# Optimization experiments

Measured on AMD Instinct MI355X. Metric: run time of the kernel, lower is better.

The kernel has to match this reference:

```python
import jax, jax.numpy as jnp
import numpy as np
from jax import lax

K = 3
STRIDE = 1
PAD = 1


def setup_inputs() -> dict:
    key = jax.random.key(0)
    k0, k1, k2, k3 = jax.random.split(key, 4)
    B, C, H, W, O = 8, 128, 64, 64, 128
    x = jax.random.normal(k0, (B, C, H, W), jnp.float32)
    # offset_conv: Conv2d(C, 2*K*K) - small init so sampled offsets stay moderate
    w_off = jax.random.normal(k1, (2 * K * K, C, K, K), jnp.float32) * 0.01
    b_off = jnp.zeros((2 * K * K,), jnp.float32)
    # deform_conv main weight, kaiming-ish scale
    w_def = jax.random.normal(k2, (O, C, K, K), jnp.float32) * (1.0 / np.sqrt(C * K * K))
    b_def = jax.random.normal(k3, (O,), jnp.float32) * 0.01
    return {"x": x, "w_off": w_off, "b_off": b_off, "w_def": w_def, "b_def": b_def}


def _conv2d(x, w, b, stride, pad):
    y = lax.conv_general_dilated(
        x, w, window_strides=(stride, stride), padding=[(pad, pad), (pad, pad)],
        dimension_numbers=("NCHW", "OIHW", "NCHW"))
    return y + b[None, :, None, None]


def _bilinear_sample(x, py, px):
    """x: [B,C,Hin,Win]; py,px: [B,KK,H,W] -> [B,C,KK,H,W] with zero padding."""
    B, C, Hin, Win = x.shape
    iy0f = jnp.floor(py)
    ix0f = jnp.floor(px)
    wy = py - iy0f  # grad of floor is 0, so d(wy)/d(py) = 1 (matches deform conv)
    wx = px - ix0f
    iy0 = iy0f.astype(jnp.int32)
    ix0 = ix0f.astype(jnp.int32)

    def gather(iy, ix):
        valid = (iy >= 0) & (iy < Hin) & (ix >= 0) & (ix < Win)
        iyc = jnp.clip(iy, 0, Hin - 1)
        ixc = jnp.clip(ix, 0, Win - 1)
        g = jax.vmap(lambda xb, a, b: xb[:, a, b])(x, iyc, ixc)  # [B,C,KK,H,W]
        return g * valid[:, None].astype(x.dtype)

    v00 = gather(iy0, ix0)
    v01 = gather(iy0, ix0 + 1)
    v10 = gather(iy0 + 1, ix0)
    v11 = gather(iy0 + 1, ix0 + 1)
    wy_ = wy[:, None]
    wx_ = wx[:, None]
    return (v00 * (1 - wy_) * (1 - wx_) + v01 * (1 - wy_) * wx_
            + v10 * wy_ * (1 - wx_) + v11 * wy_ * wx_)


def reference(x, w_off, b_off, w_def, b_def):
    B, C, H, W = x.shape
    O = w_def.shape[0]
    KK = K * K
    # 1) standard conv predicting offsets: [B, 2*KK, Hout, Wout]
    offsets = _conv2d(x, w_off, b_off, STRIDE, PAD)
    Hout, Wout = offsets.shape[2], offsets.shape[3]
    # torchvision layout: interleaved (dy, dx) per kernel tap
    off = offsets.reshape(B, KK, 2, Hout, Wout)
    off_y, off_x = off[:, :, 0], off[:, :, 1]  # [B,KK,Hout,Wout]
    # 2) base sampling grid per kernel tap
    kys, kxs = jnp.meshgrid(jnp.arange(K), jnp.arange(K), indexing="ij")
    kys = kys.reshape(KK).astype(jnp.float32)
    kxs = kxs.reshape(KK).astype(jnp.float32)
    hs = (jnp.arange(Hout) * STRIDE - PAD).astype(jnp.float32)
    ws = (jnp.arange(Wout) * STRIDE - PAD).astype(jnp.float32)
    base_y = hs[None, :, None] + kys[:, None, None]  # [KK,Hout,1]
    base_x = ws[None, None, :] + kxs[:, None, None]  # [KK,1,Wout]
    py = base_y[None] + off_y  # [B,KK,Hout,Wout]
    px = base_x[None] + off_x
    # 3) gather bilinear-sampled patches then dense contraction (im2col GEMM)
    sampled = _bilinear_sample(x, py, px)  # [B,C,KK,Hout,Wout]
    out = jnp.einsum("bckhw,ock->bohw", sampled, w_def.reshape(O, C, KK))
    return out + b_def[None, :, None, None]
```

## Files before the change

kernel.cpp:

```cpp
#include <hip/hip_runtime.h>
#include <hip/hip_bf16.h>

#define BB 8
#define CC 128
#define HH 64
#define WW 64
#define OO 128
#define NJ 18
#define HW 4096

typedef unsigned short u16;
typedef unsigned int u32;
typedef __attribute__((ext_vector_type(8))) __bf16 bf16x8;
typedef __attribute__((ext_vector_type(4))) float f32x4;

__device__ __forceinline__ u16 f2bf(float f) {
    u32 u = __float_as_uint(f);
    u += 0x7fffu + ((u >> 16) & 1u);
    return (u16)(u >> 16);
}
__device__ __forceinline__ float bflo(u32 u) { return __uint_as_float(u << 16); }
__device__ __forceinline__ float bfhi(u32 u) { return __uint_as_float(u & 0xffff0000u); }
__device__ __forceinline__ u32 pk2bf(float s0, float s1) {
    union { __hip_bfloat162 h; u32 u; } cv;
    cv.h = __float22bfloat162_rn(make_float2(s0, s1));
    return cv.u;
}

__global__ __launch_bounds__(256)
void k_xT(const float* __restrict__ x, u16* __restrict__ xT) {
    __shared__ float tile[64][129];
    const int t = threadIdx.x;
    const int b = blockIdx.x >> 6;
    const int hw0 = (blockIdx.x & 63) << 6;
    const float* xb = x + (size_t)b * CC * HW + hw0;
    const int tw = t & 63, tc = t >> 6;
#pragma unroll
    for (int r = 0; r < 32; ++r) {
        int c = r * 4 + tc;
        tile[tw][c] = xb[c * HW + tw];
    }
    __syncthreads();
    u16* dst = xT + ((size_t)b * HW + hw0) * CC;
#pragma unroll
    for (int r = 0; r < 4; ++r) {
        int item = t + (r << 8);
        int seg = item & 15, hw = item >> 4;
        union { u32 d[4]; uint4 v; } p;
#pragma unroll
        for (int i = 0; i < 4; ++i)
            p.d[i] = pk2bf(tile[hw][seg * 8 + 2 * i], tile[hw][seg * 8 + 2 * i + 1]);
        *(uint4*)&dst[hw * CC + seg * 8] = p.v;
    }
}

__global__ void k_prep(const float* __restrict__ w_def,
                       const float* __restrict__ w_off,
                       u16* __restrict__ wT, u16* __restrict__ wA) {
    int idx = blockIdx.x * 256 + threadIdx.x;
    if (idx < 9 * OO * CC) {
        int c = idx & 127, o = (idx >> 7) & 127, kk = idx >> 14;
        wT[idx] = f2bf(w_def[(o * CC + c) * 9 + kk]);
    }
    if (idx < 32 * 1152) {
        int k = idx % 1152, j = idx / 1152;
        int q = k >> 7, c = k & 127;
        wA[idx] = (j < NJ) ? f2bf(w_off[(j * CC + c) * 9 + q]) : (u16)0;
    }
}

__global__ __launch_bounds__(256, 2)
void k_off(const u16* __restrict__ xT, const u16* __restrict__ wA,
           const float* __restrict__ b_off, float* __restrict__ offs) {
    __shared__ u16 s_x[198 * 128];
    const int t = threadIdx.x, lane = t & 63, wv = t >> 6;
    const int posl = lane & 15, kg = lane >> 4;
    const int b = blockIdx.x & 7, h = blockIdx.x >> 3;

    for (int it = t; it < 3168; it += 256) {
        int seg = it & 15, pix = it >> 4;
        int r = pix / 66, wp = pix - r * 66;
        int y = h - 1 + r, w = wp - 1;
        uint4 v = make_uint4(0, 0, 0, 0);
        if (y >= 0 && y < HH && w >= 0 && w < WW)
            v = *(const uint4*)&xT[((size_t)(b * HW) + y * WW + w) * CC + seg * 8];
        *(uint4*)&s_x[pix * 128 + ((seg ^ (pix & 15)) * 8)] = v;
    }
    __syncthreads();

    f32x4 acc0 = {0.f, 0.f, 0.f, 0.f}, acc1 = {0.f, 0.f, 0.f, 0.f};
    for (int q = 0; q < 9; ++q) {
        int qy = q / 3, qx = q - qy * 3;
        int pix = qy * 66 + (wv * 16 + posl) + qx;
        int prow = pix * 128, pxor = pix & 15;
#pragma unroll
        for (int ki = 0; ki < 4; ++ki) {
            int ks = q * 4 + ki;
            int cidx = ki * 4 + kg;
            bf16x8 bfr = *(const bf16x8*)&s_x[prow + ((cidx ^ pxor) * 8)];
            bf16x8 a0 = *(const bf16x8*)&wA[posl * 1152 + ks * 32 + kg * 8];
            bf16x8 a1 = *(const bf16x8*)&wA[(16 + posl) * 1152 + ks * 32 + kg * 8];
            acc0 = __builtin_amdgcn_mfma_f32_16x16x32_bf16(a0, bfr, acc0, 0, 0, 0);
            acc1 = __builtin_amdgcn_mfma_f32_16x16x32_bf16(a1, bfr, acc1, 0, 0, 0);
        }
    }
    const int pos = wv * 16 + posl;
#pragma unroll
    for (int r = 0; r < 4; ++r) {
        int j = kg * 4 + r;
        offs[(b * NJ + j) * HW + h * WW + pos] = acc0[r] + b_off[j];
    }
#pragma unroll
    for (int r = 0; r < 4; ++r) {
        int j = 16 + kg * 4 + r;
        if (j < NJ) offs[(b * NJ + j) * HW + h * WW + pos] = acc1[r] + b_off[j];
    }
}

__global__ __launch_bounds__(256, 2)
void k_main(const u16* __restrict__ xT, const float* __restrict__ offs,
            const u16* __restrict__ wT, const float* __restrict__ b_def,
            float* __restrict__ out) {
    __shared__ u16 s_samp[2][64 * 128];

    const int t = threadIdx.x, lane = t & 63, wv = t >> 6;
    const int posl = lane & 15, kg = lane >> 4;
    const int b = blockIdx.x & 7;
    const int h = blockIdx.x >> 3;
    const char* xb = (const char*)xT + (size_t)b * (HW * CC * 2);

    const int gpos = t >> 2;
    const int segsub = t & 3;
    const int pxor = gpos & 15;
    const int slotbase = gpos * 128;

    float oyv[9], oxv[9];
#pragma unroll
    for (int kk = 0; kk < 9; ++kk) {
        oyv[kk] = offs[(b * NJ + 2 * kk) * HW + h * WW + gpos];
        oxv[kk] = offs[(b * NJ + 2 * kk + 1) * HW + h * WW + gpos];
    }

    auto coords = [&](int kk, float oy, float ox, float4& cw, int4& co) {
        int ky = kk / 3, kx = kk - ky * 3;
        float py = (float)(h - 1 + ky) + oy;
        float px = (float)(gpos - 1 + kx) + ox;
        float fy = floorf(py), fx = floorf(px);
        int iy0 = (int)fy, ix0 = (int)fx;
        float wy = py - fy, wx = px - fx;
        int iy1 = iy0 + 1, ix1 = ix0 + 1;
        float my0 = (iy0 >= 0 && iy0 < HH) ? 1.0f : 0.0f;
        float my1 = (iy1 >= 0 && iy1 < HH) ? 1.0f : 0.0f;
        float mx0 = (ix0 >= 0 && ix0 < WW) ? 1.0f : 0.0f;
        float mx1 = (ix1 >= 0 && ix1 < WW) ? 1.0f : 0.0f;
        int iy0c = min(max(iy0, 0), HH - 1), iy1c = min(max(iy1, 0), HH - 1);
        int ix0c = min(max(ix0, 0), WW - 1), ix1c = min(max(ix1, 0), WW - 1);
        float wy1 = 1.0f - wy, wx1 = 1.0f - wx;
        cw = make_float4(my0 * mx0 * wy1 * wx1, my0 * mx1 * wy1 * wx,
                         my1 * mx0 * wy  * wx1, my1 * mx1 * wy  * wx);
        co = make_int4((iy0c * WW + ix0c) << 8, (iy0c * WW + ix1c) << 8,
                       (iy1c * WW + ix0c) << 8, (iy1c * WW + ix1c) << 8);
    };
    auto issue_gather = [&](const int4 co, uint4 q[4][4]) {
#pragma unroll
        for (int j = 0; j < 4; ++j) {
            const int sb = (segsub + 4 * j) * 16;
            q[j][0] = *(const uint4*)(xb + co.x + sb);
            q[j][1] = *(const uint4*)(xb + co.y + sb);
            q[j][2] = *(const uint4*)(xb + co.z + sb);
            q[j][3] = *(const uint4*)(xb + co.w + sb);
        }
    };
    auto interp_store = [&](const float4 cw, uint4 q[4][4], int p) {
#pragma unroll
        for (int j = 0; j < 4; ++j) {
            const int seg = segsub + 4 * j;
            const u32* u00 = (const u32*)&q[j][0];
            const u32* u01 = (const u32*)&q[j][1];
            const u32* u10 = (const u32*)&q[j][2];
            const u32* u11 = (const u32*)&q[j][3];
            union { u32 d[4]; uint4 v; } pk;
#pragma unroll
            for (int i = 0; i < 4; ++i) {
                float s0 = cw.x * bflo(u00[i]) + cw.y * bflo(u01[i])
                         + cw.z * bflo(u10[i]) + cw.w * bflo(u11[i]);
                float s1 = cw.x * bfhi(u00[i]) + cw.y * bfhi(u01[i])
                         + cw.z * bfhi(u10[i]) + cw.w * bfhi(u11[i]);
                pk.d[i] = pk2bf(s0, s1);
            }
            *(uint4*)&s_samp[p][slotbase + ((seg ^ pxor) * 8)] = pk.v;
        }
    };
    auto load_w = [&](int kk, bf16x8 wfr[4][2]) {
        const u16* wkk = wT + kk * (OO * CC);
        const int o0 = wv * 32;
#pragma unroll
        for (int ct = 0; ct < 4; ++ct)
#pragma unroll
            for (int nt = 0; nt < 2; ++nt) {
                int o = o0 + nt * 16 + posl;
                wfr[ct][nt] = *(const bf16x8*)&wkk[o * CC + ct * 32 + kg * 8];
            }
    };

    f32x4 acc[4][2];
#pragma unroll
    for (int mt = 0; mt < 4; ++mt) {
        acc[mt][0] = (f32x4){0.f, 0.f, 0.f, 0.f};
        acc[mt][1] = (f32x4){0.f, 0.f, 0.f, 0.f};
    }

    bf16x8 wA_[4][2], wB_[4][2];
    float4 cw; int4 co;
    uint4 q[4][4];
    load_w(0, wA_);
    coords(0, oyv[0], oxv[0], cw, co);
    issue_gather(co, q);
    interp_store(cw, q, 0);
    __syncthreads();

#pragma unroll
    for (int kk = 0; kk < 9; ++kk) {
        const int p = kk & 1;

        if (kk < 8) {
            load_w(kk + 1, wB_);
            coords(kk + 1, oyv[kk + 1], oxv[kk + 1], cw, co);
            issue_gather(co, q);
        }

#pragma unroll
        for (int ct = 0; ct < 4; ++ct) {
            const int chunk = ct * 4 + kg;
#pragma unroll
            for (int mt = 0; mt < 4; ++mt) {
                bf16x8 afr = *(const bf16x8*)
                    &s_samp[p][(mt * 16 + posl) * 128 + ((chunk ^ posl) * 8)];
                acc[mt][0] = __builtin_amdgcn_mfma_f32_16x16x32_bf16(
                    afr, wA_[ct][0], acc[mt][0], 0, 0, 0);
                acc[mt][1] = __builtin_amdgcn_mfma_f32_16x16x32_bf16(
                    afr, wA_[ct][1], acc[mt][1], 0, 0, 0);
            }
        }

        if (kk < 8) {
            interp_store(cw, q, p ^ 1);
            __syncthreads();
        }

#pragma unroll
        for (int ct = 0; ct < 4; ++ct) {
            wA_[ct][0] = wB_[ct][0];
            wA_[ct][1] = wB_[ct][1];
        }
    }

#pragma unroll
    for (int nt = 0; nt < 2; ++nt) {
        const int o = wv * 32 + nt * 16 + posl;
        const float bd = b_def[o];
        float* orow = out + ((b * OO + o) * HH + h) * WW;
#pragma unroll
        for (int mt = 0; mt < 4; ++mt) {
            float4 res;
            res.x = acc[mt][nt][0] + bd;
            res.y = acc[mt][nt][1] + bd;
            res.z = acc[mt][nt][2] + bd;
            res.w = acc[mt][nt][3] + bd;
            *(float4*)&orow[mt * 16 + kg * 4] = res;
        }
    }
}

extern "C" void kernel_launch(void* const* d_in, const int* in_sizes, int n_in,
                              void* d_out, int out_size, void* d_ws, size_t ws_size,
                              hipStream_t stream) {
    const float* x     = (const float*)d_in[0];
    const float* w_off = (const float*)d_in[1];
    const float* b_off = (const float*)d_in[2];
    const float* w_def = (const float*)d_in[3];
    const float* b_def = (const float*)d_in[4];
    float* out = (float*)d_out;

    float* offs = (float*)d_ws;
    u16*   xT   = (u16*)(offs + BB * NJ * HW);
    u16*   wT   = xT + (size_t)BB * HW * CC;
    u16*   wA   = wT + 9 * OO * CC;

    k_xT  <<<512, 256, 0, stream>>>(x, xT);
    k_prep<<<576, 256, 0, stream>>>(w_def, w_off, wT, wA);
    k_off <<<512, 256, 0, stream>>>(xT, wA, b_off, offs);
    k_main<<<512, 256, 0, stream>>>(xT, offs, wT, b_def, out);
}
```

Baseline: 131.7 us.

## Fuse offset conv into main deform kernel and merge prep kernels

Merges the x transpose and weight prep kernels into one launch, with the block range selecting the role. Fuses the offset convolution into the main deformable-conv kernel: each block computes its row's offsets, keeps them in shared memory (aliased over the halo tile), and then runs the gather/GEMM. This removes two kernel launches and the global round trip for the offsets. In exchange the larger shared footprint and the extra work per block may lower occupancy.

```diff
diff --git a/kernel.cpp b/kernel.cpp
--- a/kernel.cpp
+++ b/kernel.cpp
@@ -28,54 +28,60 @@
 }
 
 __global__ __launch_bounds__(256)
-void k_xT(const float* __restrict__ x, u16* __restrict__ xT) {
+void k_pre(const float* __restrict__ x, u16* __restrict__ xT,
+           const float* __restrict__ w_def, const float* __restrict__ w_off,
+           u16* __restrict__ wT, u16* __restrict__ wA) {
     __shared__ float tile[64][129];
     const int t = threadIdx.x;
-    const int b = blockIdx.x >> 6;
-    const int hw0 = (blockIdx.x & 63) << 6;
-    const float* xb = x + (size_t)b * CC * HW + hw0;
-    const int tw = t & 63, tc = t >> 6;
-#pragma unroll
-    for (int r = 0; r < 32; ++r) {
-        int c = r * 4 + tc;
-        tile[tw][c] = xb[c * HW + tw];
-    }
-    __syncthreads();
-    u16* dst = xT + ((size_t)b * HW + hw0) * CC;
-#pragma unroll
-    for (int r = 0; r < 4; ++r) {
-        int item = t + (r << 8);
-        int seg = item & 15, hw = item >> 4;
-        union { u32 d[4]; uint4 v; } p;
-#pragma unroll
-        for (int i = 0; i < 4; ++i)
-            p.d[i] = pk2bf(tile[hw][seg * 8 + 2 * i], tile[hw][seg * 8 + 2 * i + 1]);
-        *(uint4*)&dst[hw * CC + seg * 8] = p.v;
-    }
-}
-
-__global__ void k_prep(const float* __restrict__ w_def,
-                       const float* __restrict__ w_off,
-                       u16* __restrict__ wT, u16* __restrict__ wA) {
-    int idx = blockIdx.x * 256 + threadIdx.x;
-    if (idx < 9 * OO * CC) {
-        int c = idx & 127, o = (idx >> 7) & 127, kk = idx >> 14;
-        wT[idx] = f2bf(w_def[(o * CC + c) * 9 + kk]);
-    }
-    if (idx < 32 * 1152) {
-        int k = idx % 1152, j = idx / 1152;
-        int q = k >> 7, c = k & 127;
-        wA[idx] = (j < NJ) ? f2bf(w_off[(j * CC + c) * 9 + q]) : (u16)0;
+    if (blockIdx.x < 512) {
+        const int b = blockIdx.x >> 6;
+        const int hw0 = (blockIdx.x & 63) << 6;
+        const float* xb = x + (size_t)b * CC * HW + hw0;
+        const int tw = t & 63, tc = t >> 6;
+#pragma unroll
+        for (int r = 0; r < 32; ++r) {
+            int c = r * 4 + tc;
+            tile[tw][c] = xb[c * HW + tw];
+        }
+        __syncthreads();
+        u16* dst = xT + ((size_t)b * HW + hw0) * CC;
+#pragma unroll
+        for (int r = 0; r < 4; ++r) {
+            int item = t + (r << 8);
+            int seg = item & 15, hw = item >> 4;
+            union { u32 d[4]; uint4 v; } p;
+#pragma unroll
+            for (int i = 0; i < 4; ++i)
+                p.d[i] = pk2bf(tile[hw][seg * 8 + 2 * i], tile[hw][seg * 8 + 2 * i + 1]);
+            *(uint4*)&dst[hw * CC + seg * 8] = p.v;
+        }
+    } else {
+        int idx = (blockIdx.x - 512) * 256 + t;
+        if (idx < 9 * OO * CC) {
+            int c = idx & 127, o = (idx >> 7) & 127, kk = idx >> 14;
+            wT[idx] = f2bf(w_def[(o * CC + c) * 9 + kk]);
+        }
+        if (idx < 32 * 1152) {
+            int k = idx % 1152, j = idx / 1152;
+            int q = k >> 7, c = k & 127;
+            wA[idx] = (j < NJ) ? f2bf(w_off[(j * CC + c) * 9 + q]) : (u16)0;
+        }
     }
 }
 
 __global__ __launch_bounds__(256, 2)
-void k_off(const u16* __restrict__ xT, const u16* __restrict__ wA,
-           const float* __restrict__ b_off, float* __restrict__ offs) {
-    __shared__ u16 s_x[198 * 128];
+void k_fused(const u16* __restrict__ xT, const u16* __restrict__ wA,
+             const float* __restrict__ b_off, const u16* __restrict__ wT,
+             const float* __restrict__ b_def, float* __restrict__ out) {
+    __shared__ __align__(16) u16 smem[25344];
+    u16*   s_x    = smem;
+    float* s_off  = (float*)smem;
+    u16*   s_samp = smem + 4096;
+
     const int t = threadIdx.x, lane = t & 63, wv = t >> 6;
     const int posl = lane & 15, kg = lane >> 4;
     const int b = blockIdx.x & 7, h = blockIdx.x >> 3;
+    const char* xb = (const char*)xT + (size_t)b * (HW * CC * 2);
 
     for (int it = t; it < 3168; it += 256) {
         int seg = it & 15, pix = it >> 4;
@@ -88,46 +94,37 @@
     }
     __syncthreads();
 
-    f32x4 acc0 = {0.f, 0.f, 0.f, 0.f}, acc1 = {0.f, 0.f, 0.f, 0.f};
-    for (int q = 0; q < 9; ++q) {
-        int qy = q / 3, qx = q - qy * 3;
-        int pix = qy * 66 + (wv * 16 + posl) + qx;
-        int prow = pix * 128, pxor = pix & 15;
-#pragma unroll
-        for (int ki = 0; ki < 4; ++ki) {
-            int ks = q * 4 + ki;
-            int cidx = ki * 4 + kg;
-            bf16x8 bfr = *(const bf16x8*)&s_x[prow + ((cidx ^ pxor) * 8)];
-            bf16x8 a0 = *(const bf16x8*)&wA[posl * 1152 + ks * 32 + kg * 8];
-            bf16x8 a1 = *(const bf16x8*)&wA[(16 + posl) * 1152 + ks * 32 + kg * 8];
-            acc0 = __builtin_amdgcn_mfma_f32_16x16x32_bf16(a0, bfr, acc0, 0, 0, 0);
-            acc1 = __builtin_amdgcn_mfma_f32_16x16x32_bf16(a1, bfr, acc1, 0, 0, 0);
-        }
-    }
-    const int pos = wv * 16 + posl;
-#pragma unroll
-    for (int r = 0; r < 4; ++r) {
-        int j = kg * 4 + r;
-        offs[(b * NJ + j) * HW + h * WW + pos] = acc0[r] + b_off[j];
-    }
-#pragma unroll
-    for (int r = 0; r < 4; ++r) {
-        int j = 16 + kg * 4 + r;
-        if (j < NJ) offs[(b * NJ + j) * HW + h * WW + pos] = acc1[r] + b_off[j];
-    }
-}
-
-__global__ __launch_bounds__(256, 2)
-void k_main(const u16* __restrict__ xT, const float* __restrict__ offs,
-            const u16* __restrict__ wT, const float* __restrict__ b_def,
-            float* __restrict__ out) {
-    __shared__ u16 s_samp[2][64 * 128];
-
-    const int t = threadIdx.x, lane = t & 63, wv = t >> 6;
-    const int posl = lane & 15, kg = lane >> 4;
-    const int b = blockIdx.x & 7;
-    const int h = blockIdx.x >> 3;
-    const char* xb = (const char*)xT + (size_t)b * (HW * CC * 2);
+    {
+        f32x4 acc0 = {0.f, 0.f, 0.f, 0.f}, acc1 = {0.f, 0.f, 0.f, 0.f};
+        for (int qq = 0; qq < 9; ++qq) {
+            int qy = qq / 3, qx = qq - qy * 3;
+            int pix = qy * 66 + (wv * 16 + posl) + qx;
+            int prow = pix * 128, pxr = pix & 15;
+#pragma unroll
+            for (int ki = 0; ki < 4; ++ki) {
+                int ks = qq * 4 + ki;
+                int cidx = ki * 4 + kg;
+                bf16x8 bfr = *(const bf16x8*)&s_x[prow + ((cidx ^ pxr) * 8)];
+                bf16x8 a0 = *(const bf16x8*)&wA[posl * 1152 + ks * 32 + kg * 8];
+                bf16x8 a1 = *(const bf16x8*)&wA[(16 + posl) * 1152 + ks * 32 + kg * 8];
+                acc0 = __builtin_amdgcn_mfma_f32_16x16x32_bf16(a0, bfr, acc0, 0, 0, 0);
+                acc1 = __builtin_amdgcn_mfma_f32_16x16x32_bf16(a1, bfr, acc1, 0, 0, 0);
+            }
+        }
+        __syncthreads();
+        const int pos = wv * 16 + posl;
+#pragma unroll
+        for (int r = 0; r < 4; ++r) {
+            int j = kg * 4 + r;
+            s_off[j * 64 + pos] = acc0[r] + b_off[j];
+        }
+#pragma unroll
+        for (int r = 0; r < 4; ++r) {
+            int j = 16 + kg * 4 + r;
+            if (j < NJ) s_off[j * 64 + pos] = acc1[r] + b_off[j];
+        }
+    }
+    __syncthreads();
 
     const int gpos = t >> 2;
     const int segsub = t & 3;
@@ -137,8 +134,8 @@
     float oyv[9], oxv[9];
 #pragma unroll
     for (int kk = 0; kk < 9; ++kk) {
-        oyv[kk] = offs[(b * NJ + 2 * kk) * HW + h * WW + gpos];
-        oxv[kk] = offs[(b * NJ + 2 * kk + 1) * HW + h * WW + gpos];
+        oyv[kk] = s_off[(2 * kk) * 64 + gpos];
+        oxv[kk] = s_off[(2 * kk + 1) * 64 + gpos];
     }
 
     auto coords = [&](int kk, float oy, float ox, float4& cw, int4& co) {
@@ -188,7 +185,7 @@
                          + cw.z * bfhi(u10[i]) + cw.w * bfhi(u11[i]);
                 pk.d[i] = pk2bf(s0, s1);
             }
-            *(uint4*)&s_samp[p][slotbase + ((seg ^ pxor) * 8)] = pk.v;
+            *(uint4*)&s_samp[p * 8192 + slotbase + ((seg ^ pxor) * 8)] = pk.v;
         }
     };
     auto load_w = [&](int kk, bf16x8 wfr[4][2]) {
@@ -235,7 +232,7 @@
 #pragma unroll
             for (int mt = 0; mt < 4; ++mt) {
                 bf16x8 afr = *(const bf16x8*)
-                    &s_samp[p][(mt * 16 + posl) * 128 + ((chunk ^ posl) * 8)];
+                    &s_samp[p * 8192 + (mt * 16 + posl) * 128 + ((chunk ^ posl) * 8)];
                 acc[mt][0] = __builtin_amdgcn_mfma_f32_16x16x32_bf16(
                     afr, wA_[ct][0], acc[mt][0], 0, 0, 0);
                 acc[mt][1] = __builtin_amdgcn_mfma_f32_16x16x32_bf16(
@@ -282,13 +279,10 @@
     const float* b_def = (const float*)d_in[4];
     float* out = (float*)d_out;
 
-    float* offs = (float*)d_ws;
-    u16*   xT   = (u16*)(offs + BB * NJ * HW);
-    u16*   wT   = xT + (size_t)BB * HW * CC;
-    u16*   wA   = wT + 9 * OO * CC;
-
-    k_xT  <<<512, 256, 0, stream>>>(x, xT);
-    k_prep<<<576, 256, 0, stream>>>(w_def, w_off, wT, wA);
-    k_off <<<512, 256, 0, stream>>>(xT, wA, b_off, offs);
-    k_main<<<512, 256, 0, stream>>>(xT, offs, wT, b_def, out);
-}
+    u16* xT = (u16*)d_ws;
+    u16* wT = xT + (size_t)BB * HW * CC;
+    u16* wA = wT + 9 * OO * CC;
+
+    k_pre  <<<1088, 256, 0, stream>>>(x, xT, w_def, w_off, wT, wA);
+    k_fused<<< 512, 256, 0, stream>>>(xT, wA, b_off, wT, b_def, out);
+}
```

Result: faster. 128.1 us (-2.7%).
